# Optimization experiments

Measured on AMD Instinct MI355X. Metric: run time of the kernel, lower is better.

Reference implementation:

```python
import jax, jax.numpy as jnp
import numpy as np
from jax import lax

K = 3
ITERATIONS = 100
LR = 0.01
UMIN, UMAX = 0.0, 63.0
MOMENTUM = 0.7
SQRT2 = float(np.sqrt(2.0))
NDC = float(0.5 * np.log(2.0 * np.pi))  # log-normalizing constant of N(0,1)


def _gausshermite(k):
    x, w = np.polynomial.hermite.hermgauss(k)
    sh = (1, 1, 1, 1, -1)
    xn = x.reshape(sh)
    wn = (w / np.sqrt(np.pi)).reshape(sh)
    xi = np.repeat(x, k).reshape(sh)   # pairwise grid, k^2 points
    xj = np.tile(x, k).reshape(sh)
    we = (np.outer(w, w) / np.pi).reshape(sh)
    f = lambda a: jnp.asarray(a, dtype=jnp.float32)
    return f(xn), f(xi), f(xj), f(wn), f(we)

XN, XI, XJ, WN, WE = _gausshermite(K)
X22 = 2 * XN ** 2 - 1
XIJ = XI * XJ
XI2AXJ2 = XI ** 2 + XJ ** 2 - 1
XI2MXJ2 = XI ** 2 - XJ ** 2


def setup_inputs() -> dict:
    key = jax.random.key(0)
    k1, k2, k3 = jax.random.split(key, 3)
    B, H, W = 4, 256, 256
    y = jax.random.uniform(k1, (B, H, W), dtype=jnp.float32) * 63.0
    edge_weight = jax.random.normal(k2, (B, H, W, 2), dtype=jnp.float32) * 0.1
    unary = jax.random.normal(k3, (B, H, W, 2), dtype=jnp.float32) * 0.05
    return {"y": y, "edge_weight": edge_weight, "unary": unary}


def _osi2(y, edge_weight, unary):
    yi = y[..., None, None]             # [B,H,W,1,1]
    ew = edge_weight[..., None]         # [B,H,W,2,1]
    uw1 = unary[..., 0:1][..., None]    # [B,H,W,1,1]
    uw2 = unary[..., 1:2][..., None]
    mu = yi
    sigma = jnp.ones_like(mu)
    rou = ew / (jnp.max(ew) * 1.01 + 1.0)
    v = jnp.zeros(ew.shape[:3] + (4, 1), dtype=ew.dtype)

    def step(carry, _):
        mu, sigma, rou, v = carry
        # unary quadrature: [B,H,W,1,K]
        xn_pts = XN * sigma * SQRT2 + mu
        fn = xn_pts * (uw1 * xn_pts + uw2 * yi)
        fn = (fn - 3 * (NDC + jnp.log(sigma))) * WN
        # pairwise quadrature over right/down neighbors: [B,H,W,2,K^2]
        q = 1 - rou ** 2
        rtq = jnp.sqrt(q)
        s = jnp.sqrt(1 + rou) / 2
        r = jnp.sqrt(1 - rou) / 2
        z1 = (s + r) * XI + (s - r) * XJ
        z2 = (s - r) * XI + (s + r) * XJ
        o2 = jnp.concatenate([jnp.roll(sigma, -1, 1), jnp.roll(sigma, -1, 2)], axis=3)
        mu2 = jnp.concatenate([jnp.roll(mu, -1, 1), jnp.roll(mu, -1, 2)], axis=3)
        fe = ew * (z1 * sigma * SQRT2 + mu) * (z2 * o2 * SQRT2 + mu2)
        fe = (fe + (2 * NDC + jnp.log(sigma * o2) + jnp.log(q) / 2)) * WE
        # natural-gradient updates
        dmu = jnp.sum(fn * XN, -1, keepdims=True) / sigma * SQRT2
        dmu += jnp.sum(jnp.sum(fe * (z1 - rou * z2), -1, keepdims=True) / (sigma * q) * SQRT2, 3, keepdims=True)
        dmu2 = jnp.sum(fe * (z2 - rou * z1), -1, keepdims=True) / (o2 * q) * SQRT2
        dmu += jnp.roll(dmu2[..., 0:1, :], 1, 1) + jnp.roll(dmu2[..., 1:2, :], 1, 2)
        dsigma = jnp.sum(fn * X22, -1, keepdims=True) / sigma
        dsigma += jnp.sum(jnp.sum(fe * (XI2AXJ2 + XI2MXJ2 / rtq), -1, keepdims=True) / sigma, 3, keepdims=True)
        dsigma2 = jnp.sum(fe * (XI2AXJ2 - XI2MXJ2 / rtq), -1, keepdims=True) / o2
        dsigma += jnp.roll(dsigma2[..., 0:1, :], 1, 1) + jnp.roll(dsigma2[..., 1:2, :], 1, 2)
        drou = jnp.sum(fe * (2 * XIJ - rou * XI2AXJ2), -1, keepdims=True) / q
        # momentum state update with clipping
        v = MOMENTUM * v + LR * jnp.concatenate([dmu, dsigma, drou], axis=3)
        mu = jnp.clip(mu + v[..., 0:1, :], UMIN, UMAX)
        sigma = jnp.clip(sigma + v[..., 1:2, :], 0.001, 50.0)
        rou = jnp.clip(rou + v[..., 2:4, :], -0.99, 0.99)
        return (mu, sigma, rou, v), None

    (mu, sigma, rou, v), _ = lax.scan(jax.checkpoint(step), (mu, sigma, rou, v), None, length=ITERATIONS)
    return mu[..., 0, 0]


def reference(y, edge_weight, unary):
    return _osi2(y, edge_weight, unary)
```

## Files before the change

kernel.cpp:

```cpp
#include <hip/hip_runtime.h>
#include <math.h>

#define NPIX  262144
#define TILE  64
#define TS    65
#define RPT   4
#define NSTRIP 16
#define NTHR  1024
#define HALO  16

__device__ __forceinline__ float clampf(float x, float lo, float hi) {
    return fminf(fmaxf(x, lo), hi);
}
__device__ __forceinline__ float dpp_shr1(float x) {
    int i = __builtin_amdgcn_update_dpp(0, __float_as_int(x),
                                        0x138, 0xf, 0xf, false);
    return __int_as_float(i);
}
__device__ __forceinline__ float dpp_shl1(float x) {
    int i = __builtin_amdgcn_update_dpp(0, __float_as_int(x),
                                        0x130, 0xf, 0xf, false);
    return __int_as_float(i);
}

__global__ __launch_bounds__(NTHR) void tile_kernel(
    const float* __restrict__ muI, const float* __restrict__ vI,
    float* __restrict__ muO, float* __restrict__ vO,
    const float4* __restrict__ c1,
    float* __restrict__ mu_out,
    int Tl,
    int first)
{
    __shared__ float buf[2][TILE*TS];

    int tid  = threadIdx.x;
    int rg   = tid >> 6;
    int lane = tid & 63;
    int bz = blockIdx.z;
    int h0 = blockIdx.y * 32;
    int w0 = blockIdx.x * 32;
    int w  = (w0 + lane - HALO) & 255;
    int r0 = RPT*rg;

    float mu[RPT], v[RPT];
    float4 k1[RPT];
    float k2y[RPT];
    float k2x0;
    int gi[RPT];

#pragma unroll
    for (int k = 0; k < RPT; ++k) {
        int h = (h0 + r0 + k - HALO) & 255;
        gi[k] = (bz << 16) | (h << 8) | w;
        mu[k] = muI[gi[k]];
        v[k]  = first ? 0.f : vI[gi[k]];
        k1[k] = c1[gi[k]];
        k2y[k] = dpp_shr1(k1[k].w);
    }
    {
        int hu = (h0 + ((rg == 0) ? 0 : r0-1) - HALO) & 255;
        k2x0 = c1[(bz << 16) | (hu << 8) | w].z;
    }
    buf[0][r0*TS + lane]       = mu[0];
    buf[0][(r0 + 3)*TS + lane] = mu[3];
    __syncthreads();

    for (int s = 0; s < Tl; ++s) {
        const float* __restrict__ cur = buf[s & 1];
        float*       __restrict__ nxt = buf[(s & 1) ^ 1];
        int lo = 14 - Tl + s;
        int rgLo = (lo <= 0) ? 0 : ((lo + 3) >> 2);
        int rgHi = (46 + Tl - s) >> 2;
        if (rg >= rgLo && rg <= rgHi) {
            float up0 = cur[((rg == 0)        ? 0        : (r0-1))*TS + lane];
            float dnL = cur[((rg == NSTRIP-1) ? (TILE-1) : (r0+RPT))*TS + lane];
            float nmu[RPT];
#pragma unroll
            for (int k = 0; k < RPT; ++k) {
                float up = (k == 0)     ? up0 : mu[k-1];
                float dn = (k == RPT-1) ? dnL : mu[k+1];
                float lf = dpp_shr1(mu[k]);
                float rt = dpp_shl1(mu[k]);
                float4 K = k1[k];
                float K2x = (k == 0) ? k2x0 : k1[k-1].z;
                float dmu = K.x*mu[k] + K.y + K.z*dn + K.w*rt
                          + K2x*up + k2y[k]*lf;
                v[k] = 0.7f*v[k] + 0.01f*dmu;
                nmu[k] = clampf(mu[k] + v[k], 0.f, 63.f);
            }
#pragma unroll
            for (int k = 0; k < RPT; ++k) mu[k] = nmu[k];
            nxt[r0*TS + lane]       = mu[0];
            nxt[(r0 + 3)*TS + lane] = mu[3];
        }
        __syncthreads();
    }

    if (lane >= HALO && lane < HALO+32) {
#pragma unroll
        for (int k = 0; k < RPT; ++k) {
            int r = r0 + k;
            if (r >= HALO && r < HALO+32) {
                if (mu_out) {
                    mu_out[gi[k]] = mu[k];
                } else {
                    muO[gi[k]] = mu[k];
                    vO[gi[k]]  = v[k];
                }
            }
        }
    }
}

__global__ __launch_bounds__(256) void init_state_kernel(
    const float*  __restrict__ y,
    const float2* __restrict__ ew,
    const float2* __restrict__ uw,
    float* muA, float4* c1)
{
    int idx = blockIdx.x*256 + threadIdx.x;
    float2 e   = ew[idx];
    float2 uwv = uw[idx];
    float  yv  = y[idx];
    muA[idx] = yv;
    c1[idx]  = make_float4(2.f*uwv.x, uwv.y*yv, e.x, e.y);
}

extern "C" void kernel_launch(void* const* d_in, const int* in_sizes, int n_in,
                              void* d_out, int out_size, void* d_ws, size_t ws_size,
                              hipStream_t stream) {
    const float* y  = (const float*)d_in[0];
    const float* ew = (const float*)d_in[1];
    const float* uw = (const float*)d_in[2];
    float* out = (float*)d_out;
    const int N = NPIX;

    float4* c1  = (float4*)d_ws;
    float*  muA = (float*)(c1 + N);
    float*  muB = muA + N;
    float*  vA  = muB + N;
    float*  vB  = vA + N;

    hipLaunchKernelGGL(init_state_kernel, dim3(N/256), dim3(256), 0, stream,
                       y, (const float2*)ew, (const float2*)uw, muA, c1);

    static const int Tls[7] = {15, 15, 15, 15, 15, 15, 10};
    float *muI = muA, *muO = muB, *vI = vA, *vO = vB;
    for (int l = 0; l < 7; ++l) {
        float* mo = (l == 6) ? out : nullptr;
        hipLaunchKernelGGL(tile_kernel, dim3(8, 8, 4), dim3(NTHR), 0, stream,
                           muI, vI, muO, vO, c1, mo, Tls[l], (l == 0) ? 1 : 0);
        float* t;
        t = muI; muI = muO; muO = t;
        t = vI;  vI  = vO;  vO  = t;
    }
}
```

Before: 141.1 us.

## Fuse two time steps per barrier with redundant halo-row recomputation

Each strip now advances two momentum steps per shared-memory exchange by recomputing the neighbouring boundary rows (and their velocities, which are now shared via LDS) locally, halving the number of __syncthreads rounds. Mu and v state are packed into a float2 array so global loads and stores are merged, and the init kernel zeroes v, which removes the first-launch flag. The price is extra arithmetic for the two halo rows, more LDS traffic and registers per step, and an extra tail path for odd step counts.

```diff
diff --git a/kernel.cpp b/kernel.cpp
--- a/kernel.cpp
+++ b/kernel.cpp
@@ -22,16 +22,24 @@
                                         0x130, 0xf, 0xf, false);
     return __int_as_float(i);
 }
+__device__ __forceinline__ float rowstep(float mu_c, float up, float dn,
+                                         float4 K, float K2x, float K2y,
+                                         float& v) {
+    float lf = dpp_shr1(mu_c);
+    float rt = dpp_shl1(mu_c);
+    float dmu = K.x*mu_c + K.y + K.z*dn + K.w*rt + K2x*up + K2y*lf;
+    v = 0.7f*v + 0.01f*dmu;
+    return clampf(mu_c + v, 0.f, 63.f);
+}
 
 __global__ __launch_bounds__(NTHR) void tile_kernel(
-    const float* __restrict__ muI, const float* __restrict__ vI,
-    float* __restrict__ muO, float* __restrict__ vO,
+    const float2* __restrict__ muvI, float2* __restrict__ muvO,
     const float4* __restrict__ c1,
     float* __restrict__ mu_out,
-    int Tl,
-    int first)
+    int Tl)
 {
-    __shared__ float buf[2][TILE*TS];
+    __shared__ float muB[2][TILE*TS];
+    __shared__ float vB[2][2*NSTRIP*TS];
 
     int tid  = threadIdx.x;
     int rg   = tid >> 6;
@@ -43,57 +51,86 @@
     int r0 = RPT*rg;
 
     float mu[RPT], v[RPT];
-    float4 k1[RPT];
-    float k2y[RPT];
-    float k2x0;
+    float4 k1[RPT], kT, kBt;
+    float k2y[RPT], k2yT, k2yB, kzT2;
     int gi[RPT];
 
 #pragma unroll
     for (int k = 0; k < RPT; ++k) {
         int h = (h0 + r0 + k - HALO) & 255;
         gi[k] = (bz << 16) | (h << 8) | w;
-        mu[k] = muI[gi[k]];
-        v[k]  = first ? 0.f : vI[gi[k]];
+        float2 s = muvI[gi[k]];
+        mu[k] = s.x;  v[k] = s.y;
         k1[k] = c1[gi[k]];
         k2y[k] = dpp_shr1(k1[k].w);
     }
     {
-        int hu = (h0 + ((rg == 0) ? 0 : r0-1) - HALO) & 255;
-        k2x0 = c1[(bz << 16) | (hu << 8) | w].z;
+        int hT  = (h0 + ((rg == 0) ? 0 : r0-1) - HALO) & 255;
+        int hB  = (h0 + ((rg == NSTRIP-1) ? TILE-1 : r0+4) - HALO) & 255;
+        int hT2 = (h0 + ((r0 < 2) ? 0 : r0-2) - HALO) & 255;
+        kT   = c1[(bz << 16) | (hT  << 8) | w];
+        kBt  = c1[(bz << 16) | (hB  << 8) | w];
+        kzT2 = c1[(bz << 16) | (hT2 << 8) | w].z;
+        k2yT = dpp_shr1(kT.w);
+        k2yB = dpp_shr1(kBt.w);
     }
-    buf[0][r0*TS + lane]       = mu[0];
-    buf[0][(r0 + 3)*TS + lane] = mu[3];
+#pragma unroll
+    for (int k = 0; k < RPT; ++k) muB[0][(r0+k)*TS + lane] = mu[k];
+    vB[0][(2*rg)*TS + lane]   = v[0];
+    vB[0][(2*rg+1)*TS + lane] = v[3];
     __syncthreads();
 
-    for (int s = 0; s < Tl; ++s) {
-        const float* __restrict__ cur = buf[s & 1];
-        float*       __restrict__ nxt = buf[(s & 1) ^ 1];
-        int lo = 14 - Tl + s;
-        int rgLo = (lo <= 0) ? 0 : ((lo + 3) >> 2);
-        int rgHi = (46 + Tl - s) >> 2;
-        if (rg >= rgLo && rg <= rgHi) {
-            float up0 = cur[((rg == 0)        ? 0        : (r0-1))*TS + lane];
-            float dnL = cur[((rg == NSTRIP-1) ? (TILE-1) : (r0+RPT))*TS + lane];
-            float nmu[RPT];
+    int P = Tl >> 1, odd = Tl & 1;
+    int rm2 = (r0 < 2) ? 0 : r0-2;
+    int rm1 = (rg == 0) ? 0 : r0-1;
+    int rp4 = (rg == NSTRIP-1) ? TILE-1 : r0+4;
+    int rp5 = (r0+5 > TILE-1) ? TILE-1 : r0+5;
+    int sT  = (rg == 0) ? 0 : 2*rg-1;
+    int sB  = (rg == NSTRIP-1) ? 2*NSTRIP-1 : 2*rg+2;
+
+    for (int p = 0; p < P; ++p) {
+        const float* __restrict__ curM = muB[p & 1];
+        float*       __restrict__ nxtM = muB[(p & 1) ^ 1];
+        const float* __restrict__ curV = vB[p & 1];
+        float*       __restrict__ nxtV = vB[(p & 1) ^ 1];
+        int lo = 18 - Tl + 2*p, hi = 45 + Tl - 2*p;
+        if (r0+3 >= lo && r0 <= hi) {
+            float mT2 = curM[rm2*TS + lane];
+            float mT1 = curM[rm1*TS + lane];
+            float mB4 = curM[rp4*TS + lane];
+            float mB5 = curM[rp5*TS + lane];
+            float vT  = curV[sT*TS + lane];
+            float vBo = curV[sB*TS + lane];
+            float a0 = rowstep(mT1,   mT2,   mu[0], kT,    kzT2,    k2yT,   vT);
+            float a1 = rowstep(mu[0], mT1,   mu[1], k1[0], kT.z,    k2y[0], v[0]);
+            float a2 = rowstep(mu[1], mu[0], mu[2], k1[1], k1[0].z, k2y[1], v[1]);
+            float a3 = rowstep(mu[2], mu[1], mu[3], k1[2], k1[1].z, k2y[2], v[2]);
+            float a4 = rowstep(mu[3], mu[2], mB4,   k1[3], k1[2].z, k2y[3], v[3]);
+            float a5 = rowstep(mB4,   mu[3], mB5,   kBt,   k1[3].z, k2yB,   vBo);
+            mu[0] = rowstep(a1, a0, a2, k1[0], kT.z,    k2y[0], v[0]);
+            mu[1] = rowstep(a2, a1, a3, k1[1], k1[0].z, k2y[1], v[1]);
+            mu[2] = rowstep(a3, a2, a4, k1[2], k1[1].z, k2y[2], v[2]);
+            mu[3] = rowstep(a4, a3, a5, k1[3], k1[2].z, k2y[3], v[3]);
+            if (p < P-1 || odd) {
 #pragma unroll
-            for (int k = 0; k < RPT; ++k) {
-                float up = (k == 0)     ? up0 : mu[k-1];
-                float dn = (k == RPT-1) ? dnL : mu[k+1];
-                float lf = dpp_shr1(mu[k]);
-                float rt = dpp_shl1(mu[k]);
-                float4 K = k1[k];
-                float K2x = (k == 0) ? k2x0 : k1[k-1].z;
-                float dmu = K.x*mu[k] + K.y + K.z*dn + K.w*rt
-                          + K2x*up + k2y[k]*lf;
-                v[k] = 0.7f*v[k] + 0.01f*dmu;
-                nmu[k] = clampf(mu[k] + v[k], 0.f, 63.f);
+                for (int k = 0; k < RPT; ++k) nxtM[(r0+k)*TS + lane] = mu[k];
+                nxtV[(2*rg)*TS + lane]   = v[0];
+                nxtV[(2*rg+1)*TS + lane] = v[3];
             }
-#pragma unroll
-            for (int k = 0; k < RPT; ++k) mu[k] = nmu[k];
-            nxt[r0*TS + lane]       = mu[0];
-            nxt[(r0 + 3)*TS + lane] = mu[3];
         }
         __syncthreads();
+    }
+    if (odd) {
+        const float* __restrict__ curM = muB[P & 1];
+        if (r0 >= 16 && r0+3 <= 47) {
+            float mT1 = curM[rm1*TS + lane];
+            float mB4 = curM[rp4*TS + lane];
+            float a1 = rowstep(mu[0], mT1,   mu[1], k1[0], kT.z,    k2y[0], v[0]);
+            float a2 = rowstep(mu[1], mu[0], mu[2], k1[1], k1[0].z, k2y[1], v[1]);
+            float a3 = rowstep(mu[2], mu[1], mu[3], k1[2], k1[1].z, k2y[2], v[2]);
+            float a4 = rowstep(mu[3], mu[2], mB4,   k1[3], k1[2].z, k2y[3], v[3]);
+            mu[0] = a1; mu[1] = a2; mu[2] = a3; mu[3] = a4;
+        }
     }
 
     if (lane >= HALO && lane < HALO+32) {
@@ -104,8 +141,7 @@
                 if (mu_out) {
                     mu_out[gi[k]] = mu[k];
                 } else {
-                    muO[gi[k]] = mu[k];
-                    vO[gi[k]]  = v[k];
+                    muvO[gi[k]] = make_float2(mu[k], v[k]);
                 }
             }
         }
@@ -116,14 +152,14 @@
     const float*  __restrict__ y,
     const float2* __restrict__ ew,
     const float2* __restrict__ uw,
-    float* muA, float4* c1)
+    float2* muvA, float4* c1)
 {
     int idx = blockIdx.x*256 + threadIdx.x;
     float2 e   = ew[idx];
     float2 uwv = uw[idx];
     float  yv  = y[idx];
-    muA[idx] = yv;
-    c1[idx]  = make_float4(2.f*uwv.x, uwv.y*yv, e.x, e.y);
+    muvA[idx] = make_float2(yv, 0.f);
+    c1[idx]   = make_float4(2.f*uwv.x, uwv.y*yv, e.x, e.y);
 }
 
 extern "C" void kernel_launch(void* const* d_in, const int* in_sizes, int n_in,
@@ -135,23 +171,19 @@
     float* out = (float*)d_out;
     const int N = NPIX;
 
-    float4* c1  = (float4*)d_ws;
-    float*  muA = (float*)(c1 + N);
-    float*  muB = muA + N;
-    float*  vA  = muB + N;
-    float*  vB  = vA + N;
+    float4* c1   = (float4*)d_ws;
+    float2* muvA = (float2*)(c1 + N);
+    float2* muvB = muvA + N;
 
     hipLaunchKernelGGL(init_state_kernel, dim3(N/256), dim3(256), 0, stream,
-                       y, (const float2*)ew, (const float2*)uw, muA, c1);
+                       y, (const float2*)ew, (const float2*)uw, muvA, c1);
 
     static const int Tls[7] = {15, 15, 15, 15, 15, 15, 10};
-    float *muI = muA, *muO = muB, *vI = vA, *vO = vB;
+    float2 *muvI = muvA, *muvO = muvB;
     for (int l = 0; l < 7; ++l) {
         float* mo = (l == 6) ? out : nullptr;
         hipLaunchKernelGGL(tile_kernel, dim3(8, 8, 4), dim3(NTHR), 0, stream,
-                           muI, vI, muO, vO, c1, mo, Tls[l], (l == 0) ? 1 : 0);
-        float* t;
-        t = muI; muI = muO; muO = t;
-        t = vI;  vI  = vO;  vO  = t;
+                           muvI, muvO, c1, mo, Tls[l]);
+        float2* t = muvI; muvI = muvO; muvO = t;
     }
 }
```

New measurement: 143.0 us. About the same (+1.4%).

## Pack stencil math with v_pk_fma, interleave mu/v state, rebalance temporal blocks

Applied to the files above, without the earlier changes.

Rewrites the per-step stencil update to process row pairs with packed FP32 FMA instructions, halving VALU instruction count. Stores mu and velocity as interleaved float2 to cut separate loads/stores, and removes the trailing barrier. Changes the temporal blocking schedule to use 16 steps per launch, which pushes the halo to its limit and risks boundary contamination.

```diff
diff --git a/kernel.cpp b/kernel.cpp
--- a/kernel.cpp
+++ b/kernel.cpp
@@ -9,8 +9,28 @@
 #define NTHR  1024
 #define HALO  16
 
-__device__ __forceinline__ float clampf(float x, float lo, float hi) {
-    return fminf(fmaxf(x, lo), hi);
+typedef float v2f __attribute__((ext_vector_type(2)));
+
+__device__ __forceinline__ v2f pk_fma(v2f a, v2f b, v2f c) {
+    v2f d;
+    asm("v_pk_fma_f32 %0, %1, %2, %3" : "=v"(d) : "v"(a), "v"(b), "v"(c));
+    return d;
+}
+__device__ __forceinline__ v2f pk_mul(v2f a, v2f b) {
+    v2f d;
+    asm("v_pk_mul_f32 %0, %1, %2" : "=v"(d) : "v"(a), "v"(b));
+    return d;
+}
+__device__ __forceinline__ v2f pk_add(v2f a, v2f b) {
+    v2f d;
+    asm("v_pk_add_f32 %0, %1, %2" : "=v"(d) : "v"(a), "v"(b));
+    return d;
+}
+__device__ __forceinline__ v2f pk_clamp(v2f a) {
+    v2f d;
+    d.x = fminf(fmaxf(a.x, 0.f), 63.f);
+    d.y = fminf(fmaxf(a.y, 0.f), 63.f);
+    return d;
 }
 __device__ __forceinline__ float dpp_shr1(float x) {
     int i = __builtin_amdgcn_update_dpp(0, __float_as_int(x),
@@ -24,8 +44,7 @@
 }
 
 __global__ __launch_bounds__(NTHR) void tile_kernel(
-    const float* __restrict__ muI, const float* __restrict__ vI,
-    float* __restrict__ muO, float* __restrict__ vO,
+    const float2* __restrict__ muvI, float2* __restrict__ muvO,
     const float4* __restrict__ c1,
     float* __restrict__ mu_out,
     int Tl,
@@ -44,26 +63,41 @@
 
     float mu[RPT], v[RPT];
     float4 k1[RPT];
-    float k2y[RPT];
-    float k2x0;
     int gi[RPT];
 
 #pragma unroll
     for (int k = 0; k < RPT; ++k) {
         int h = (h0 + r0 + k - HALO) & 255;
         gi[k] = (bz << 16) | (h << 8) | w;
-        mu[k] = muI[gi[k]];
-        v[k]  = first ? 0.f : vI[gi[k]];
+        float2 s = muvI[gi[k]];
+        mu[k] = s.x;
+        v[k]  = first ? 0.f : s.y;
         k1[k] = c1[gi[k]];
-        k2y[k] = dpp_shr1(k1[k].w);
     }
+    float k2x0;
     {
         int hu = (h0 + ((rg == 0) ? 0 : r0-1) - HALO) & 255;
         k2x0 = c1[(bz << 16) | (hu << 8) | w].z;
     }
-    buf[0][r0*TS + lane]       = mu[0];
-    buf[0][(r0 + 3)*TS + lane] = mu[3];
+
+    v2f pmA = {mu[0], mu[3]}, pmB = {mu[1], mu[2]};
+    v2f pvA = {v[0],  v[3]},  pvB = {v[1],  v[2]};
+    v2f KxA = {k1[0].x, k1[3].x}, KxB = {k1[1].x, k1[2].x};
+    v2f KyA = {k1[0].y, k1[3].y}, KyB = {k1[1].y, k1[2].y};
+    v2f KzA = {k1[0].z, k1[3].z}, KzB = {k1[1].z, k1[2].z};
+    v2f KwA = {k1[0].w, k1[3].w}, KwB = {k1[1].w, k1[2].w};
+    v2f K2xA = {k2x0,    k1[2].z}, K2xB = {k1[0].z, k1[1].z};
+    v2f K2yA = {dpp_shr1(k1[0].w), dpp_shr1(k1[3].w)};
+    v2f K2yB = {dpp_shr1(k1[1].w), dpp_shr1(k1[2].w)};
+    const v2f C07  = {0.7f, 0.7f};
+    const v2f C001 = {0.01f, 0.01f};
+
+    buf[0][r0*TS + lane]       = pmA.x;
+    buf[0][(r0 + 3)*TS + lane] = pmA.y;
     __syncthreads();
+
+    int rm1 = (rg == 0)        ? 0      : r0-1;
+    int rp4 = (rg == NSTRIP-1) ? TILE-1 : r0+4;
 
     for (int s = 0; s < Tl; ++s) {
         const float* __restrict__ cur = buf[s & 1];
@@ -72,40 +106,49 @@
         int rgLo = (lo <= 0) ? 0 : ((lo + 3) >> 2);
         int rgHi = (46 + Tl - s) >> 2;
         if (rg >= rgLo && rg <= rgHi) {
-            float up0 = cur[((rg == 0)        ? 0        : (r0-1))*TS + lane];
-            float dnL = cur[((rg == NSTRIP-1) ? (TILE-1) : (r0+RPT))*TS + lane];
-            float nmu[RPT];
-#pragma unroll
-            for (int k = 0; k < RPT; ++k) {
-                float up = (k == 0)     ? up0 : mu[k-1];
-                float dn = (k == RPT-1) ? dnL : mu[k+1];
-                float lf = dpp_shr1(mu[k]);
-                float rt = dpp_shl1(mu[k]);
-                float4 K = k1[k];
-                float K2x = (k == 0) ? k2x0 : k1[k-1].z;
-                float dmu = K.x*mu[k] + K.y + K.z*dn + K.w*rt
-                          + K2x*up + k2y[k]*lf;
-                v[k] = 0.7f*v[k] + 0.01f*dmu;
-                nmu[k] = clampf(mu[k] + v[k], 0.f, 63.f);
-            }
-#pragma unroll
-            for (int k = 0; k < RPT; ++k) mu[k] = nmu[k];
-            nxt[r0*TS + lane]       = mu[0];
-            nxt[(r0 + 3)*TS + lane] = mu[3];
+            float up0 = cur[rm1*TS + lane];
+            float dnL = cur[rp4*TS + lane];
+            v2f upA = {up0,   pmB.y};
+            v2f dnA = {pmB.x, dnL};
+            v2f lfA = {dpp_shr1(pmA.x), dpp_shr1(pmA.y)};
+            v2f rtA = {dpp_shl1(pmA.x), dpp_shl1(pmA.y)};
+            v2f d = pk_fma(KxA, pmA, KyA);
+            d = pk_fma(KzA, dnA, d);
+            d = pk_fma(KwA, rtA, d);
+            d = pk_fma(K2xA, upA, d);
+            d = pk_fma(K2yA, lfA, d);
+            pvA = pk_fma(pvA, C07, pk_mul(C001, d));
+            v2f nmA = pk_clamp(pk_add(pmA, pvA));
+            nxt[r0*TS + lane]       = nmA.x;
+            nxt[(r0 + 3)*TS + lane] = nmA.y;
+            v2f upB = {pmA.x, pmB.x};
+            v2f dnB = {pmB.y, pmA.y};
+            v2f lfB = {dpp_shr1(pmB.x), dpp_shr1(pmB.y)};
+            v2f rtB = {dpp_shl1(pmB.x), dpp_shl1(pmB.y)};
+            v2f e = pk_fma(KxB, pmB, KyB);
+            e = pk_fma(KzB, dnB, e);
+            e = pk_fma(KwB, rtB, e);
+            e = pk_fma(K2xB, upB, e);
+            e = pk_fma(K2yB, lfB, e);
+            pvB = pk_fma(pvB, C07, pk_mul(C001, e));
+            v2f nmB = pk_clamp(pk_add(pmB, pvB));
+            pmA = nmA;
+            pmB = nmB;
         }
-        __syncthreads();
+        if (s + 1 < Tl) __syncthreads();
     }
 
     if (lane >= HALO && lane < HALO+32) {
+        float muO[RPT] = {pmA.x, pmB.x, pmB.y, pmA.y};
+        float vO_[RPT] = {pvA.x, pvB.x, pvB.y, pvA.y};
 #pragma unroll
         for (int k = 0; k < RPT; ++k) {
             int r = r0 + k;
             if (r >= HALO && r < HALO+32) {
                 if (mu_out) {
-                    mu_out[gi[k]] = mu[k];
+                    mu_out[gi[k]] = muO[k];
                 } else {
-                    muO[gi[k]] = mu[k];
-                    vO[gi[k]]  = v[k];
+                    muvO[gi[k]] = make_float2(muO[k], vO_[k]);
                 }
             }
         }
@@ -116,14 +159,14 @@
     const float*  __restrict__ y,
     const float2* __restrict__ ew,
     const float2* __restrict__ uw,
-    float* muA, float4* c1)
+    float2* muvA, float4* c1)
 {
     int idx = blockIdx.x*256 + threadIdx.x;
     float2 e   = ew[idx];
     float2 uwv = uw[idx];
     float  yv  = y[idx];
-    muA[idx] = yv;
-    c1[idx]  = make_float4(2.f*uwv.x, uwv.y*yv, e.x, e.y);
+    muvA[idx] = make_float2(yv, 0.f);
+    c1[idx]   = make_float4(2.f*uwv.x, uwv.y*yv, e.x, e.y);
 }
 
 extern "C" void kernel_launch(void* const* d_in, const int* in_sizes, int n_in,
@@ -135,23 +178,19 @@
     float* out = (float*)d_out;
     const int N = NPIX;
 
-    float4* c1  = (float4*)d_ws;
-    float*  muA = (float*)(c1 + N);
-    float*  muB = muA + N;
-    float*  vA  = muB + N;
-    float*  vB  = vA + N;
+    float4* c1   = (float4*)d_ws;
+    float2* muvA = (float2*)(c1 + N);
+    float2* muvB = muvA + N;
 
     hipLaunchKernelGGL(init_state_kernel, dim3(N/256), dim3(256), 0, stream,
-                       y, (const float2*)ew, (const float2*)uw, muA, c1);
+                       y, (const float2*)ew, (const float2*)uw, muvA, c1);
 
-    static const int Tls[7] = {15, 15, 15, 15, 15, 15, 10};
-    float *muI = muA, *muO = muB, *vI = vA, *vO = vB;
+    static const int Tls[7] = {16, 16, 16, 16, 16, 16, 4};
+    float2 *muvI = muvA, *muvO = muvB;
     for (int l = 0; l < 7; ++l) {
         float* mo = (l == 6) ? out : nullptr;
         hipLaunchKernelGGL(tile_kernel, dim3(8, 8, 4), dim3(NTHR), 0, stream,
-                           muI, vI, muO, vO, c1, mo, Tls[l], (l == 0) ? 1 : 0);
-        float* t;
-        t = muI; muI = muO; muO = t;
-        t = vI;  vI  = vO;  vO  = t;
+                           muvI, muvO, c1, mo, Tls[l], (l == 0) ? 1 : 0);
+        float2* t = muvI; muvI = muvO; muvO = t;
     }
 }
```

Result: faster. 133.5 us (-5.4%).
